# Kernel tuning notes

Hardware: AMD Instinct MI355X
Metric: run time of the kernel (lower is better)

The kernel has to match this reference:

```python
import jax, jax.numpy as jnp
import numpy as np

N = 131072   # num_nodes
E = 262144   # events in the batch
D = 128      # memory_dim
R = 128      # raw_msg_dim
T = 32       # time_dim


def setup_inputs() -> dict:
    key = jax.random.key(0)
    ks = jax.random.split(key, 16)
    s = 0.05
    return {
        "memory": jax.random.normal(ks[0], (N, D), jnp.float32) * s,
        "raw_msg": jax.random.normal(ks[1], (E, R), jnp.float32) * s,
        "time_w": jax.random.normal(ks[2], (T,), jnp.float32) * s,
        "time_b": jax.random.normal(ks[3], (T,), jnp.float32) * s,
        "W_msg_s": jax.random.normal(ks[4], (D, 2 * D + R + T), jnp.float32) * s,
        "b_msg_s": jax.random.normal(ks[5], (D,), jnp.float32) * s,
        "W_msg_d": jax.random.normal(ks[6], (D, 2 * D + R + T), jnp.float32) * s,
        "b_msg_d": jax.random.normal(ks[7], (D,), jnp.float32) * s,
        "W_ih": jax.random.normal(ks[8], (3 * D, D), jnp.float32) * s,
        "W_hh": jax.random.normal(ks[9], (3 * D, D), jnp.float32) * s,
        "b_ih": jax.random.normal(ks[10], (3 * D,), jnp.float32) * s,
        "b_hh": jax.random.normal(ks[11], (3 * D,), jnp.float32) * s,
        "src": jax.random.randint(ks[12], (E,), 0, N, jnp.int32),
        "dst": jax.random.randint(ks[13], (E,), 0, N, jnp.int32),
        "t": jax.random.randint(ks[14], (E,), 0, 100000, jnp.int32),
        "last_update": jax.random.randint(ks[15], (N,), 0, 50000, jnp.int32),
    }


def _time_enc(t_rel, time_w, time_b):
    # TimeEncoder: cos(Linear(t)) ; t_rel: [E] float -> [E, T]
    return jnp.cos(t_rel[:, None] * time_w[None, :] + time_b[None, :])


def _message(mem_a, mem_b, raw_msg, t_enc, W, b):
    # message MLP on concat(mem_src, mem_dst, raw_msg, t_enc)
    x = jnp.concatenate([mem_a, mem_b, raw_msg, t_enc], axis=-1)  # [E, 2D+R+T]
    return jax.nn.relu(x @ W.T + b)


def _forward(memory, raw_msg, time_w, time_b, W_msg_s, b_msg_s, W_msg_d, b_msg_d,
             W_ih, W_hh, b_ih, b_hh, src, dst, t, last_update):
    tf = t.astype(jnp.float32)
    lu = last_update.astype(jnp.float32)
    mem_s = memory[src]  # gather [E, D]
    mem_d = memory[dst]

    # source-side messages (stored under key src): t_rel = t - last_update[src]
    t_enc_s = _time_enc(tf - lu[src], time_w, time_b)
    msg_s = _message(mem_s, mem_d, raw_msg, t_enc_s, W_msg_s, b_msg_s)
    # dest-side messages (stored under key dst, src/dst swapped)
    t_enc_d = _time_enc(tf - lu[dst], time_w, time_b)
    msg_d = _message(mem_d, mem_s, raw_msg, t_enc_d, W_msg_d, b_msg_d)

    # scatter mean-aggregate messages onto their owner node
    seg = jnp.concatenate([src, dst], axis=0)          # [2E]
    vals = jnp.concatenate([msg_s, msg_d], axis=0)     # [2E, D]
    sums = jax.ops.segment_sum(vals, seg, num_segments=N)
    cnt = jax.ops.segment_sum(jnp.ones((2 * E,), jnp.float32), seg, num_segments=N)
    aggr = sums / jnp.maximum(cnt, 1.0)[:, None]       # [N, D]

    # GRUCell(aggr, memory)
    gi = aggr @ W_ih.T + b_ih
    gh = memory @ W_hh.T + b_hh
    i_r, i_z, i_n = jnp.split(gi, 3, axis=-1)
    h_r, h_z, h_n = jnp.split(gh, 3, axis=-1)
    r = jax.nn.sigmoid(i_r + h_r)
    z = jax.nn.sigmoid(i_z + h_z)
    n = jnp.tanh(i_n + r * h_n)
    new_memory = (1.0 - z) * n + z * memory

    # scatter-max timestamps (pyg scatter reduce='max' fills empty slots with 0)
    tt = jnp.concatenate([t, t], axis=0)
    seg_max = jax.ops.segment_max(tt, seg, num_segments=N)
    new_last_update = jnp.where(cnt > 0, seg_max, jnp.zeros((), jnp.int32))
    return new_memory, new_last_update


def reference(memory, raw_msg, time_w, time_b, W_msg_s, b_msg_s, W_msg_d, b_msg_d,
              W_ih, W_hh, b_ih, b_hh, src, dst, t, last_update):
    return _forward(memory, raw_msg, time_w, time_b, W_msg_s, b_msg_s, W_msg_d,
                    b_msg_d, W_ih, W_hh, b_ih, b_hh, src, dst, t, last_update)
```

## Files before the change

### kernel.cpp

```cpp
#include <hip/hip_runtime.h>
#include <cstdint>
#include <cstddef>

#define NN 131072
#define EE 262144

typedef __attribute__((ext_vector_type(8))) short bf16x8;
typedef __attribute__((ext_vector_type(4))) float f32x4;

__device__ __forceinline__ unsigned short f2bf(float f) {
    unsigned int u = __builtin_bit_cast(unsigned int, f);
    u += 0x7FFFu + ((u >> 16) & 1u);
    return (unsigned short)(u >> 16);
}
__device__ __forceinline__ float bf2f(unsigned short s) {
    unsigned int u = ((unsigned int)s) << 16;
    return __builtin_bit_cast(float, u);
}
__device__ __forceinline__ float sigmoidf_(float x) { return 1.0f / (1.0f + __expf(-x)); }
__device__ __forceinline__ float tanhf_(float x) {
    float ax = fabsf(x);
    float e = __expf(-2.0f * ax);
    return copysignf((1.0f - e) / (1.0f + e), x);
}
__device__ __forceinline__ bf16x8 pack8(const float* f) {
    bf16x8 o;
#pragma unroll
    for (int i = 0; i < 8; ++i) o[i] = (short)f2bf(f[i]);
    return o;
}

__device__ __forceinline__ float wmsg_val(int n, int k, const float* Ws, const float* Wd) {
    if (n < 128) {
        return (k < 416) ? Ws[n * 416 + k] : 0.0f;
    } else {
        int m = n - 128;
        if (k < 128)       return Wd[m * 416 + 128 + k];
        else if (k < 256)  return Wd[m * 416 + (k - 128)];
        else if (k < 384)  return Wd[m * 416 + k];
        else if (k < 416)  return 0.0f;
        else               return Wd[m * 416 + 384 + (k - 416)];
    }
}
__device__ __forceinline__ float wgru_val(int j, int k, const float* Wih, const float* Whh) {
    if (j < 256)      return (k < 128) ? Wih[j * 128 + k] : Whh[j * 128 + (k - 128)];
    else if (j < 384) return (k < 128) ? Wih[j * 128 + k] : 0.0f;
    else              return (k < 128) ? 0.0f : Whh[(j - 128) * 128 + (k - 128)];
}

__global__ void k_prep_msgfrag(const float* __restrict__ Ws, const float* __restrict__ Wd,
                               const float* __restrict__ bs, const float* __restrict__ bd,
                               unsigned short* __restrict__ Wmf, float* __restrict__ bm) {
    int b = blockIdx.x;
    int c = b >> 4, nt = b & 15;
    int lane = threadIdx.x;
    int col0 = lane & 15, q = lane >> 4;
    int n = nt * 16 + col0;
    float f[8];
#pragma unroll
    for (int j = 0; j < 8; ++j) f[j] = wmsg_val(n, c * 32 + q * 8 + j, Ws, Wd);
    ((bf16x8*)Wmf)[(size_t)b * 64 + lane] = pack8(f);
    if (b == 0)
        for (int i = lane; i < 256; i += 64) bm[i] = (i < 128) ? bs[i] : bd[i - 128];
}

__global__ void k_prep_grufrag(const float* __restrict__ Wih, const float* __restrict__ Whh,
                               const float* __restrict__ bih, const float* __restrict__ bhh,
                               unsigned short* __restrict__ Wgf, float* __restrict__ bg) {
    int b = blockIdx.x;
    int c = b >> 5, nt = b & 31;
    int lane = threadIdx.x;
    int col0 = lane & 15, q = lane >> 4;
    int j0 = nt * 16 + col0;
    float f[8];
#pragma unroll
    for (int j = 0; j < 8; ++j) f[j] = wgru_val(j0, c * 32 + q * 8 + j, Wih, Whh);
    ((bf16x8*)Wgf)[(size_t)b * 64 + lane] = pack8(f);
    if (b == 0)
        for (int i = lane; i < 512; i += 64)
            bg[i] = (i < 256) ? (bih[i] + bhh[i]) : ((i < 384) ? bih[i] : bhh[i - 128]);
}

__global__ void k_memconv(const float* __restrict__ in, unsigned short* __restrict__ outp) {
    int gid = blockIdx.x * 256 + threadIdx.x;
    const float4 v = ((const float4*)in)[gid];
    ushort4 o;
    o.x = f2bf(v.x); o.y = f2bf(v.y); o.z = f2bf(v.z); o.w = f2bf(v.w);
    *(ushort4*)(outp + (size_t)gid * 4) = o;
}

__global__ void k_pre(const int* __restrict__ t, const int* __restrict__ src,
                      const int* __restrict__ dst, const int* __restrict__ lu,
                      float* __restrict__ trel_s, float* __restrict__ trel_d,
                      int* cnt, int* lu_tmp) {
    int e = blockIdx.x * 256 + threadIdx.x;
    int s = src[e], d = dst[e], tv = t[e];
    trel_s[e] = (float)(tv - lu[s]);
    trel_d[e] = (float)(tv - lu[d]);
    atomicAdd(&cnt[s], 1);
    atomicAdd(&cnt[d], 1);
    atomicMax(&lu_tmp[s], tv);
    atomicMax(&lu_tmp[d], tv);
}

__global__ void k_scan1(const int* __restrict__ cnt, int* __restrict__ bsum) {
    __shared__ int red[256];
    int tid = threadIdx.x;
    red[tid] = cnt[blockIdx.x * 256 + tid];
    __syncthreads();
    for (int s = 128; s > 0; s >>= 1) {
        if (tid < s) red[tid] += red[tid + s];
        __syncthreads();
    }
    if (tid == 0) bsum[blockIdx.x] = red[0];
}
__global__ void k_scan2(const int* __restrict__ bsum, int* __restrict__ boff) {
    __shared__ int sb[512];
    int tid = threadIdx.x;
    int v = bsum[tid];
    sb[tid] = v;
    __syncthreads();
    for (int d = 1; d < 512; d <<= 1) {
        int u = (tid >= d) ? sb[tid - d] : 0;
        __syncthreads();
        sb[tid] += u;
        __syncthreads();
    }
    boff[tid] = sb[tid] - v;
}
__global__ void k_scan3(const int* __restrict__ cnt, const int* __restrict__ boff,
                        int* __restrict__ off, int* __restrict__ cursor) {
    __shared__ int sb[256];
    int tid = threadIdx.x;
    int i = blockIdx.x * 256 + tid;
    int v = cnt[i];
    sb[tid] = v;
    __syncthreads();
    for (int d = 1; d < 256; d <<= 1) {
        int u = (tid >= d) ? sb[tid - d] : 0;
        __syncthreads();
        sb[tid] += u;
        __syncthreads();
    }
    int o = boff[blockIdx.x] + sb[tid] - v;
    off[i] = o;
    cursor[i] = o;
}
__global__ void k_fill(const int* __restrict__ src, const int* __restrict__ dst,
                       int* cursor, int* __restrict__ pos2) {
    int e2 = blockIdx.x * 256 + threadIdx.x;
    int node = (e2 < EE) ? src[e2] : dst[e2 - EE];
    pos2[e2] = atomicAdd(&cursor[node], 1);
}

__launch_bounds__(256, 2)
__global__ void k_msg(const unsigned short* __restrict__ memb,
                      const float* __restrict__ raw,
                      const float* __restrict__ trel_s,
                      const float* __restrict__ trel_d,
                      const unsigned short* __restrict__ Wmf,
                      const float* __restrict__ bm,
                      const int* __restrict__ src, const int* __restrict__ dst,
                      const int* __restrict__ pos2,
                      const float* __restrict__ tw, const float* __restrict__ tb,
                      unsigned short* __restrict__ msg) {
    __shared__ int s_idx[128], d_idx[128], s_pos[128], d_pos[128];
    __shared__ float s_tw[32], s_tb[32];
    __shared__ __align__(16) unsigned short As[2][128 * 40];

    const int tid = threadIdx.x;
    const int e0 = blockIdx.x * 128;
    if (tid < 128) { s_idx[tid] = src[e0 + tid]; s_pos[tid] = pos2[e0 + tid]; }
    else { d_idx[tid - 128] = dst[e0 + tid - 128]; d_pos[tid - 128] = pos2[EE + e0 + tid - 128]; }
    if (tid < 32)       s_tw[tid] = tw[tid];
    else if (tid < 64)  s_tb[tid - 32] = tb[tid - 32];
    __syncthreads();

    const int lane = tid & 63, w = tid >> 6;
    const int col0 = lane & 15, q = lane >> 4;

    auto stage = [&](int cc) {
        unsigned short* A = As[cc & 1];
        if (cc < 8) {
#pragma unroll
            for (int i = 0; i < 2; ++i) {
                int lin = tid + 256 * i;
                int row = lin >> 2, seg = lin & 3;
                int node = (cc < 4) ? s_idx[row] : d_idx[row];
                bf16x8 v = *(const bf16x8*)(memb + (size_t)node * 128 + (cc & 3) * 32 + seg * 8);
                *(bf16x8*)&A[row * 40 + seg * 8] = v;
            }
        } else if (cc < 12) {
#pragma unroll
            for (int i = 0; i < 4; ++i) {
                int lin = tid + 256 * i;
                int row = lin >> 3, seg = lin & 7;
                const float4 v = *(const float4*)(raw + (size_t)(e0 + row) * 128 + (cc - 8) * 32 + seg * 4);
                ushort4 o;
                o.x = f2bf(v.x); o.y = f2bf(v.y); o.z = f2bf(v.z); o.w = f2bf(v.w);
                *(ushort4*)&A[row * 40 + seg * 4] = o;
            }
        } else {
            int row = tid >> 1, half = tid & 1;
            float tr = (cc == 12) ? trel_s[e0 + row] : trel_d[e0 + row];
            float f[16];
#pragma unroll
            for (int j2 = 0; j2 < 16; ++j2) {
                int jj = half * 16 + j2;
                f[j2] = __cosf(tr * s_tw[jj] + s_tb[jj]);
            }
            *(bf16x8*)&A[row * 40 + half * 16] = pack8(&f[0]);
            *(bf16x8*)&A[row * 40 + half * 16 + 8] = pack8(&f[8]);
        }
    };

    f32x4 acc[8][4];
#pragma unroll
    for (int a = 0; a < 8; ++a)
#pragma unroll
        for (int b = 0; b < 4; ++b)
#pragma unroll
            for (int i = 0; i < 4; ++i) acc[a][b][i] = 0.0f;

    stage(0);
    __syncthreads();

    for (int c = 0; c < 14; ++c) {
        bf16x8 bfr[4];
        const bf16x8* Wc = (const bf16x8*)Wmf + (size_t)c * 16 * 64;
#pragma unroll
        for (int nl = 0; nl < 4; ++nl)
            bfr[nl] = Wc[(w * 4 + nl) * 64 + lane];
        const unsigned short* A = As[c & 1];
        bf16x8 afr[8];
#pragma unroll
        for (int mt = 0; mt < 8; ++mt)
            afr[mt] = *(const bf16x8*)&A[(mt * 16 + col0) * 40 + q * 8];
        if (c < 13) stage(c + 1);
#pragma unroll
        for (int mt = 0; mt < 8; ++mt)
#pragma unroll
            for (int nl = 0; nl < 4; ++nl)
                acc[mt][nl] = __builtin_amdgcn_mfma_f32_16x16x32_bf16(afr[mt], bfr[nl], acc[mt][nl], 0, 0, 0);
        __syncthreads();
    }

#pragma unroll
    for (int nl = 0; nl < 4; ++nl) {
        int j = (w * 4 + nl) * 16 + col0;
        float bv = bm[j];
        int feat = j & 127;
        bool is_s = (j < 128);
#pragma unroll
        for (int mt = 0; mt < 8; ++mt) {
#pragma unroll
            for (int r = 0; r < 4; ++r) {
                int ev = mt * 16 + q * 4 + r;
                float v = fmaxf(acc[mt][nl][r] + bv, 0.0f);
                int pos = is_s ? s_pos[ev] : d_pos[ev];
                msg[(size_t)pos * 128 + feat] = f2bf(v);
            }
        }
    }
}

__launch_bounds__(256, 3)
__global__ void k_gru(const unsigned short* __restrict__ msg,
                      const int* __restrict__ off, const int* __restrict__ cnt,
                      const float* __restrict__ memory,
                      const unsigned short* __restrict__ Wgf,
                      const float* __restrict__ bg,
                      float* __restrict__ out) {
    __shared__ __align__(16) unsigned short Xs[32 * 264];

    const int tid = threadIdx.x;
    const int n0 = blockIdx.x * 32;

    {
        int g = tid >> 3, sub = tid & 7;
        int node = n0 + g;
        int beg = off[node], cn = cnt[node];
        float a[16];
#pragma unroll
        for (int i = 0; i < 16; ++i) a[i] = 0.0f;
        for (int m = 0; m < cn; ++m) {
            const bf16x8* p = (const bf16x8*)(msg + (size_t)(beg + m) * 128 + sub * 16);
            bf16x8 v0 = p[0], v1 = p[1];
#pragma unroll
            for (int k = 0; k < 8; ++k) {
                a[k]     += bf2f((unsigned short)v0[k]);
                a[8 + k] += bf2f((unsigned short)v1[k]);
            }
        }
        float inv = 1.0f / (float)(cn > 1 ? cn : 1);
#pragma unroll
        for (int i = 0; i < 16; ++i) a[i] *= inv;
        *(bf16x8*)&Xs[g * 264 + sub * 16] = pack8(&a[0]);
        *(bf16x8*)&Xs[g * 264 + sub * 16 + 8] = pack8(&a[8]);
        float f[16];
        const float4* mp = (const float4*)(memory + (size_t)node * 128 + sub * 16);
#pragma unroll
        for (int s = 0; s < 4; ++s) {
            float4 v = mp[s];
            f[s * 4 + 0] = v.x; f[s * 4 + 1] = v.y; f[s * 4 + 2] = v.z; f[s * 4 + 3] = v.w;
        }
        *(bf16x8*)&Xs[g * 264 + 128 + sub * 16] = pack8(&f[0]);
        *(bf16x8*)&Xs[g * 264 + 128 + sub * 16 + 8] = pack8(&f[8]);
    }
    __syncthreads();

    const int lane = tid & 63, w = tid >> 6;
    const int col0 = lane & 15, q = lane >> 4;

    f32x4 acc[2][4][2];
#pragma unroll
    for (int a = 0; a < 2; ++a)
#pragma unroll
        for (int g = 0; g < 4; ++g)
#pragma unroll
            for (int f = 0; f < 2; ++f)
#pragma unroll
                for (int i = 0; i < 4; ++i) acc[a][g][f][i] = 0.0f;

#pragma unroll
    for (int c = 0; c < 8; ++c) {
        bf16x8 bfr[4][2];
        const bf16x8* Wc = (const bf16x8*)Wgf + (size_t)c * 32 * 64;
#pragma unroll
        for (int g = 0; g < 4; ++g)
#pragma unroll
            for (int fh = 0; fh < 2; ++fh)
                bfr[g][fh] = Wc[(8 * g + 2 * w + fh) * 64 + lane];
        bf16x8 afr[2];
#pragma unroll
        for (int mt = 0; mt < 2; ++mt)
            afr[mt] = *(const bf16x8*)&Xs[(mt * 16 + col0) * 264 + c * 32 + q * 8];
#pragma unroll
        for (int mt = 0; mt < 2; ++mt)
#pragma unroll
            for (int g = 0; g < 4; ++g)
#pragma unroll
                for (int fh = 0; fh < 2; ++fh)
                    acc[mt][g][fh] = __builtin_amdgcn_mfma_f32_16x16x32_bf16(afr[mt], bfr[g][fh], acc[mt][g][fh], 0, 0, 0);
    }

#pragma unroll
    for (int fh = 0; fh < 2; ++fh) {
        int feat = w * 32 + fh * 16 + col0;
        float b_r = bg[feat], b_z = bg[128 + feat], b_in = bg[256 + feat], b_hn = bg[384 + feat];
#pragma unroll
        for (int mt = 0; mt < 2; ++mt) {
#pragma unroll
            for (int r = 0; r < 4; ++r) {
                int node = n0 + mt * 16 + q * 4 + r;
                float rr = sigmoidf_(acc[mt][0][fh][r] + b_r);
                float zz = sigmoidf_(acc[mt][1][fh][r] + b_z);
                float nn = tanhf_((acc[mt][2][fh][r] + b_in) + rr * (acc[mt][3][fh][r] + b_hn));
                float h = memory[(size_t)node * 128 + feat];
                out[(size_t)node * 128 + feat] = (1.0f - zz) * nn + zz * h;
            }
        }
    }
}

__global__ void k_lu(const int* __restrict__ lu_tmp, float* __restrict__ outp) {
    int i = blockIdx.x * 256 + threadIdx.x;
    outp[i] = (float)lu_tmp[i];
}

extern "C" void kernel_launch(void* const* d_in, const int* in_sizes, int n_in,
                              void* d_out, int out_size, void* d_ws, size_t ws_size,
                              hipStream_t stream) {
    const float* memory = (const float*)d_in[0];
    const float* raw    = (const float*)d_in[1];
    const float* tw     = (const float*)d_in[2];
    const float* tb     = (const float*)d_in[3];
    const float* Wms    = (const float*)d_in[4];
    const float* bms    = (const float*)d_in[5];
    const float* Wmd    = (const float*)d_in[6];
    const float* bmd    = (const float*)d_in[7];
    const float* Wih    = (const float*)d_in[8];
    const float* Whh    = (const float*)d_in[9];
    const float* bih    = (const float*)d_in[10];
    const float* bhh    = (const float*)d_in[11];
    const int* src = (const int*)d_in[12];
    const int* dst = (const int*)d_in[13];
    const int* t   = (const int*)d_in[14];
    const int* lu  = (const int*)d_in[15];

    char* ws = (char*)d_ws;
    size_t ob = 0;
    unsigned short* memb = (unsigned short*)(ws + ob); ob += (size_t)NN * 128 * 2;
    unsigned short* msg  = (unsigned short*)(ws + ob); ob += (size_t)2 * EE * 128 * 2;
    float* trel_s        = (float*)(ws + ob);          ob += (size_t)EE * 4;
    float* trel_d        = (float*)(ws + ob);          ob += (size_t)EE * 4;
    int* cnt             = (int*)(ws + ob);            ob += (size_t)NN * 4;
    int* off             = (int*)(ws + ob);            ob += (size_t)NN * 4;
    int* cursor          = (int*)(ws + ob);            ob += (size_t)NN * 4;
    int* lu_tmp          = (int*)(ws + ob);            ob += (size_t)NN * 4;
    int* pos2            = (int*)(ws + ob);            ob += (size_t)2 * EE * 4;
    int* bsum            = (int*)(ws + ob);            ob += 512 * 4;
    int* boff            = (int*)(ws + ob);            ob += 512 * 4;
    unsigned short* Wmf  = (unsigned short*)(ws + ob); ob += (size_t)14 * 16 * 64 * 8 * 2;
    float* bm            = (float*)(ws + ob);          ob += 256 * 4;
    unsigned short* Wgf  = (unsigned short*)(ws + ob); ob += (size_t)8 * 32 * 64 * 8 * 2;
    float* bg            = (float*)(ws + ob);          ob += 512 * 4;

    float* out = (float*)d_out;

    hipMemsetAsync(cnt, 0, (size_t)NN * 4, stream);
    hipMemsetAsync(lu_tmp, 0, (size_t)NN * 4, stream);

    k_prep_msgfrag<<<14 * 16, 64, 0, stream>>>(Wms, Wmd, bms, bmd, Wmf, bm);
    k_prep_grufrag<<<8 * 32, 64, 0, stream>>>(Wih, Whh, bih, bhh, Wgf, bg);
    k_memconv<<<(NN * 128 / 4) / 256, 256, 0, stream>>>(memory, memb);
    k_pre<<<EE / 256, 256, 0, stream>>>(t, src, dst, lu, trel_s, trel_d, cnt, lu_tmp);
    k_scan1<<<512, 256, 0, stream>>>(cnt, bsum);
    k_scan2<<<1, 512, 0, stream>>>(bsum, boff);
    k_scan3<<<512, 256, 0, stream>>>(cnt, boff, off, cursor);
    k_fill<<<2 * EE / 256, 256, 0, stream>>>(src, dst, cursor, pos2);
    k_msg<<<EE / 128, 256, 0, stream>>>(memb, raw, trel_s, trel_d, Wmf, bm, src, dst, pos2, tw, tb, msg);
    k_gru<<<NN / 32, 256, 0, stream>>>(msg, off, cnt, memory, Wgf, bg, out);
    k_lu<<<NN / 256, 256, 0, stream>>>(lu_tmp, out + (size_t)NN * 128);
}
```

Baseline: 573.9 us.

## Halve message tile to 64 events and stage output through LDS for vector stores

The message kernel now handles 64 events per block instead of 128, with half the accumulators and LDS, and asks for 3 blocks per SM for higher occupancy. The epilogue writes relu outputs into a swizzled LDS scratch per wave, then issues 16-byte vector stores to the scattered message rows instead of scattered 2-byte stores. Weight fragments are now reloaded for twice as many blocks, and the epilogue relies on per-wave lgkmcnt waits instead of barriers.

Result: slower. 589.0 us (+2.6%).

```diff
diff --git a/kernel.cpp b/kernel.cpp
--- a/kernel.cpp
+++ b/kernel.cpp
@@ -153,7 +153,7 @@
     pos2[e2] = atomicAdd(&cursor[node], 1);
 }
 
-__launch_bounds__(256, 2)
+__launch_bounds__(256, 3)
 __global__ void k_msg(const unsigned short* __restrict__ memb,
                       const float* __restrict__ raw,
                       const float* __restrict__ trel_s,
@@ -164,16 +164,16 @@
                       const int* __restrict__ pos2,
                       const float* __restrict__ tw, const float* __restrict__ tb,
                       unsigned short* __restrict__ msg) {
-    __shared__ int s_idx[128], d_idx[128], s_pos[128], d_pos[128];
+    __shared__ int s_idx[64], d_idx[64], s_pos[64], d_pos[64];
     __shared__ float s_tw[32], s_tb[32];
-    __shared__ __align__(16) unsigned short As[2][128 * 40];
+    __shared__ __align__(16) unsigned short As[2][64 * 40];
 
     const int tid = threadIdx.x;
-    const int e0 = blockIdx.x * 128;
-    if (tid < 128) { s_idx[tid] = src[e0 + tid]; s_pos[tid] = pos2[e0 + tid]; }
-    else { d_idx[tid - 128] = dst[e0 + tid - 128]; d_pos[tid - 128] = pos2[EE + e0 + tid - 128]; }
-    if (tid < 32)       s_tw[tid] = tw[tid];
-    else if (tid < 64)  s_tb[tid - 32] = tb[tid - 32];
+    const int e0 = blockIdx.x * 64;
+    if (tid < 64)        { s_idx[tid] = src[e0 + tid];            s_pos[tid] = pos2[e0 + tid]; }
+    else if (tid < 128)  { d_idx[tid - 64] = dst[e0 + tid - 64];  d_pos[tid - 64] = pos2[EE + e0 + tid - 64]; }
+    else if (tid < 160)  s_tw[tid - 128] = tw[tid - 128];
+    else if (tid < 192)  s_tb[tid - 160] = tb[tid - 160];
     __syncthreads();
 
     const int lane = tid & 63, w = tid >> 6;
@@ -182,17 +182,13 @@
     auto stage = [&](int cc) {
         unsigned short* A = As[cc & 1];
         if (cc < 8) {
+            int row = tid >> 2, seg = tid & 3;
+            int node = (cc < 4) ? s_idx[row] : d_idx[row];
+            bf16x8 v = *(const bf16x8*)(memb + (size_t)node * 128 + (cc & 3) * 32 + seg * 8);
+            *(bf16x8*)&A[row * 40 + seg * 8] = v;
+        } else if (cc < 12) {
 #pragma unroll
             for (int i = 0; i < 2; ++i) {
-                int lin = tid + 256 * i;
-                int row = lin >> 2, seg = lin & 3;
-                int node = (cc < 4) ? s_idx[row] : d_idx[row];
-                bf16x8 v = *(const bf16x8*)(memb + (size_t)node * 128 + (cc & 3) * 32 + seg * 8);
-                *(bf16x8*)&A[row * 40 + seg * 8] = v;
-            }
-        } else if (cc < 12) {
-#pragma unroll
-            for (int i = 0; i < 4; ++i) {
                 int lin = tid + 256 * i;
                 int row = lin >> 3, seg = lin & 7;
                 const float4 v = *(const float4*)(raw + (size_t)(e0 + row) * 128 + (cc - 8) * 32 + seg * 4);
@@ -201,22 +197,21 @@
                 *(ushort4*)&A[row * 40 + seg * 4] = o;
             }
         } else {
-            int row = tid >> 1, half = tid & 1;
+            int row = tid >> 2, quarter = tid & 3;
             float tr = (cc == 12) ? trel_s[e0 + row] : trel_d[e0 + row];
-            float f[16];
-#pragma unroll
-            for (int j2 = 0; j2 < 16; ++j2) {
-                int jj = half * 16 + j2;
+            float f[8];
+#pragma unroll
+            for (int j2 = 0; j2 < 8; ++j2) {
+                int jj = quarter * 8 + j2;
                 f[j2] = __cosf(tr * s_tw[jj] + s_tb[jj]);
             }
-            *(bf16x8*)&A[row * 40 + half * 16] = pack8(&f[0]);
-            *(bf16x8*)&A[row * 40 + half * 16 + 8] = pack8(&f[8]);
+            *(bf16x8*)&A[row * 40 + quarter * 8] = pack8(f);
         }
     };
 
-    f32x4 acc[8][4];
-#pragma unroll
-    for (int a = 0; a < 8; ++a)
+    f32x4 acc[4][4];
+#pragma unroll
+    for (int a = 0; a < 4; ++a)
 #pragma unroll
         for (int b = 0; b < 4; ++b)
 #pragma unroll
@@ -232,35 +227,48 @@
         for (int nl = 0; nl < 4; ++nl)
             bfr[nl] = Wc[(w * 4 + nl) * 64 + lane];
         const unsigned short* A = As[c & 1];
-        bf16x8 afr[8];
-#pragma unroll
-        for (int mt = 0; mt < 8; ++mt)
+        bf16x8 afr[4];
+#pragma unroll
+        for (int mt = 0; mt < 4; ++mt)
             afr[mt] = *(const bf16x8*)&A[(mt * 16 + col0) * 40 + q * 8];
         if (c < 13) stage(c + 1);
 #pragma unroll
-        for (int mt = 0; mt < 8; ++mt)
+        for (int mt = 0; mt < 4; ++mt)
 #pragma unroll
             for (int nl = 0; nl < 4; ++nl)
                 acc[mt][nl] = __builtin_amdgcn_mfma_f32_16x16x32_bf16(afr[mt], bfr[nl], acc[mt][nl], 0, 0, 0);
         __syncthreads();
     }
 
-#pragma unroll
-    for (int nl = 0; nl < 4; ++nl) {
-        int j = (w * 4 + nl) * 16 + col0;
-        float bv = bm[j];
-        int feat = j & 127;
-        bool is_s = (j < 128);
-#pragma unroll
-        for (int mt = 0; mt < 8; ++mt) {
+    unsigned short* scr = &As[0][0] + w * 1280;
+    const bool is_s = (w < 2);
+#pragma unroll
+    for (int mt = 0; mt < 4; ++mt) {
+#pragma unroll
+        for (int nl = 0; nl < 4; ++nl) {
+            int j = (w * 4 + nl) * 16 + col0;
+            float bv = bm[j];
+            int gl = nl * 2 + (col0 >> 3);
+            int ci = col0 & 7;
 #pragma unroll
             for (int r = 0; r < 4; ++r) {
-                int ev = mt * 16 + q * 4 + r;
+                int rr = q * 4 + r;
                 float v = fmaxf(acc[mt][nl][r] + bv, 0.0f);
-                int pos = is_s ? s_pos[ev] : d_pos[ev];
-                msg[(size_t)pos * 128 + feat] = f2bf(v);
+                scr[rr * 80 + ((gl + rr) & 7) * 8 + ci] = f2bf(v);
             }
         }
+        asm volatile("s_waitcnt lgkmcnt(0)" ::: "memory");
+        {
+            int rr2 = lane & 15, p = lane >> 4;
+            int ev = mt * 16 + rr2;
+            int pos = is_s ? s_pos[ev] : d_pos[ev];
+            bf16x8 v0 = *(const bf16x8*)&scr[rr2 * 80 + (((2 * p)     + rr2) & 7) * 8];
+            bf16x8 v1 = *(const bf16x8*)&scr[rr2 * 80 + (((2 * p + 1) + rr2) & 7) * 8];
+            unsigned short* dstp = msg + (size_t)pos * 128 + (w & 1) * 64 + p * 16;
+            *(bf16x8*)dstp = v0;
+            *(bf16x8*)(dstp + 8) = v1;
+        }
+        asm volatile("s_waitcnt lgkmcnt(0)" ::: "memory");
     }
 }
 
@@ -419,7 +427,7 @@
     k_scan2<<<1, 512, 0, stream>>>(bsum, boff);
     k_scan3<<<512, 256, 0, stream>>>(cnt, boff, off, cursor);
     k_fill<<<2 * EE / 256, 256, 0, stream>>>(src, dst, cursor, pos2);
-    k_msg<<<EE / 128, 256, 0, stream>>>(memb, raw, trel_s, trel_d, Wmf, bm, src, dst, pos2, tw, tb, msg);
+    k_msg<<<EE / 64, 256, 0, stream>>>(memb, raw, trel_s, trel_d, Wmf, bm, src, dst, pos2, tw, tb, msg);
     k_gru<<<NN / 32, 256, 0, stream>>>(msg, off, cnt, memory, Wgf, bg, out);
     k_lu<<<NN / 256, 256, 0, stream>>>(lu_tmp, out + (size_t)NN * 128);
 }
```
